# Optimization experiments

Hardware: AMD Instinct MI355X
Metric: run time of the kernel (lower is better)

The kernel has to match this reference:

```python
import jax, jax.numpy as jnp
import numpy as np

CIN, COUT, K = 64, 64, 3
ALPHA = 8.3
STRIDE, PAD, DIL = 1, 1, 1
B, H = 8, 128


def _unfold(x, k, dilation, padding, stride):
    # torch.nn.functional.unfold: output feature order is (C, kh, kw)
    x = jnp.pad(x, ((0, 0), (0, 0), (padding, padding), (padding, padding)))
    b, c, h, w = x.shape
    eff = dilation * (k - 1) + 1
    oh = (h - eff) // stride + 1
    ow = (w - eff) // stride + 1
    cols = []
    for i in range(k):
        for j in range(k):
            cols.append(x[:, :, i * dilation:i * dilation + stride * oh:stride,
                              j * dilation:j * dilation + stride * ow:stride])
    p = jnp.stack(cols, axis=2)          # [B, C, k*k, oh, ow]
    return p.reshape(b, c * k * k, oh * ow)


def setup_inputs() -> dict:
    key = jax.random.key(0)
    k1, k2, k3, k4 = jax.random.split(key, 4)
    image = jax.random.normal(k1, (B, CIN, H, H), dtype=jnp.float32)
    depth = jax.random.uniform(k2, (B, 1, H, H), dtype=jnp.float32)
    weight = jax.random.normal(k3, (COUT, CIN, K, K), dtype=jnp.float32) * 0.05
    bias = jax.random.normal(k4, (COUT,), dtype=jnp.float32) * 0.05
    return {"image": image, "depth": depth, "weight": weight, "bias": bias}


def reference(image, depth, weight, bias):
    # im2col of the image: [B, L, Cin*k*k]
    patches = _unfold(image, K, DIL, PAD, STRIDE).transpose(0, 2, 1)
    b, L, _ = patches.shape
    # depth is repeat()'d to Cin channels in the original; the unfolded depth
    # columns therefore tile the single-channel patch Cin times. Exploit that:
    dpatch = _unfold(depth, K, DIL, PAD, STRIDE).transpose(0, 2, 1)  # [B, L, k*k]
    # original centre index: int((Cin*k*k)/2); within the tiled patch this is
    # position (Cin*k*k//2) % (k*k) of the single-channel patch
    centre_idx = (CIN * K * K // 2) % (K * K)
    centre = dpatch[:, :, centre_idx:centre_idx + 1]
    sim = jnp.exp(-ALPHA * jnp.abs(dpatch - centre))  # [B, L, k*k]
    # modulate per kernel offset (broadcast over channels == tiled similarity)
    modulated = patches.reshape(b, L, CIN, K * K) * sim[:, :, None, :]
    out = jnp.einsum('blck,ock->blo', modulated, weight.reshape(COUT, CIN, K * K))
    out = out + bias
    osz = (image.shape[-1] + 2 * PAD - DIL * (K - 1) - 1) // STRIDE + 1
    return out.transpose(0, 2, 1).reshape(b, COUT, osz, osz)
```

## Files before the change

### kernel.cpp

```cpp
#include <hip/hip_runtime.h>
#include <hip/hip_bf16.h>

#define BATCH 8
#define CIN   64
#define COUT  64
#define HH    128
#define WW    128
#define ALPHA 8.3f
#define TPX   64
#define YPB   4
#define XW    66

typedef __attribute__((ext_vector_type(8))) short short8;
typedef __attribute__((ext_vector_type(4))) float f32x4;

__device__ __forceinline__ int img_idx(int r, int x, int c) {
    return (((r * XW + x) << 6) + c) ^ ((x & 7) << 3);
}

__global__ __launch_bounds__(256)
void transpose_w(const float* __restrict__ w, __hip_bfloat16* __restrict__ wt) {
    int i = blockIdx.x * 256 + threadIdx.x;
    if (i >= 9 * 64 * 64) return;
    int c = i & 63;
    int o = (i >> 6) & 63;
    int tap = i >> 12;
    wt[i] = __float2bfloat16(w[(o * 64 + c) * 9 + tap]);
}

__global__ __launch_bounds__(256)
void depthconv_mfma(const float* __restrict__ image,
                    const float* __restrict__ depth,
                    const float* __restrict__ bias,
                    const short* __restrict__ wt,
                    float* __restrict__ out) {
    __shared__ short s_img[3 * XW * 64];
    __shared__ float s_d[3][XW];
    __shared__ float s_sim[9][TPX];

    const int tid = threadIdx.x;
    const int bid = blockIdx.x;
    const int yg = bid & 31;
    const int xt = (bid >> 5) & 1;
    const int b  = bid >> 6;
    const int x0 = xt * TPX;

    const int lane = tid & 63;
    const int wid  = tid >> 6;
    const int l15  = lane & 15;
    const int lq   = lane >> 4;
    const int o_base = wid * 16;

    short8 wfrag[9][2];
    #pragma unroll
    for (int tap = 0; tap < 9; ++tap)
        #pragma unroll
        for (int h = 0; h < 2; ++h)
            wfrag[tap][h] = *(const short8*)&wt[(tap * 64 + o_base + l15) * 64 + h * 32 + lq * 8];

    float bias_v[4];
    #pragma unroll
    for (int r = 0; r < 4; ++r) bias_v[r] = bias[o_base + lq * 4 + r];

    for (int yi = 0; yi < YPB; ++yi) {
        const int y = yg * YPB + yi;
        __syncthreads();

        for (int i = tid; i < 3 * XW * 32; i += 256) {
            int x  = i % XW;
            int rr = (i / XW) % 3;
            int c  = (i / (3 * XW)) * 2;
            int gy = y + rr - 1, gx = x0 - 1 + x;
            float v0 = 0.f, v1 = 0.f;
            if ((unsigned)gy < HH && (unsigned)gx < WW) {
                const float* p = &image[((b * CIN + c) * HH + gy) * WW + gx];
                v0 = p[0];
                v1 = p[HH * WW];
            }
            __hip_bfloat162 pk = __float22bfloat162_rn(float2{v0, v1});
            *(__hip_bfloat162*)&s_img[img_idx(rr, x, c)] = pk;
        }
        for (int i = tid; i < 3 * XW; i += 256) {
            int x = i % XW, rr = i / XW;
            int gy = y + rr - 1, gx = x0 - 1 + x;
            float v = 0.f;
            if ((unsigned)gy < HH && (unsigned)gx < WW)
                v = depth[(b * HH + gy) * WW + gx];
            s_d[rr][x] = v;
        }
        __syncthreads();

        for (int i = tid; i < 9 * TPX; i += 256) {
            int p = i & 63, tap = i >> 6;
            int ri = tap / 3, dj = tap % 3;
            float dt = s_d[ri][p + dj];
            float dc = s_d[0][p];
            s_sim[tap][p] = __expf(-ALPHA * fabsf(dt - dc));
        }
        __syncthreads();

        f32x4 acc[4];
        #pragma unroll
        for (int nt = 0; nt < 4; ++nt) acc[nt] = f32x4{0.f, 0.f, 0.f, 0.f};

        #pragma unroll
        for (int tap = 0; tap < 9; ++tap) {
            const int ri = tap / 3, dj = tap % 3;
            float sv[4];
            #pragma unroll
            for (int nt = 0; nt < 4; ++nt) sv[nt] = s_sim[tap][nt * 16 + l15];
            #pragma unroll
            for (int nt = 0; nt < 4; ++nt) {
                const int xi = nt * 16 + l15 + dj;
                short8 b0 = *(const short8*)&s_img[img_idx(ri, xi, lq * 8)];
                f32x4 tmp = __builtin_amdgcn_mfma_f32_16x16x32_bf16(
                    wfrag[tap][0], b0, (f32x4){0.f, 0.f, 0.f, 0.f}, 0, 0, 0);
                short8 b1 = *(const short8*)&s_img[img_idx(ri, xi, 32 + lq * 8)];
                tmp = __builtin_amdgcn_mfma_f32_16x16x32_bf16(
                    wfrag[tap][1], b1, tmp, 0, 0, 0);
                #pragma unroll
                for (int r = 0; r < 4; ++r)
                    acc[nt][r] = fmaf(sv[nt], tmp[r], acc[nt][r]);
            }
        }

        #pragma unroll
        for (int nt = 0; nt < 4; ++nt) {
            int px = x0 + nt * 16 + l15;
            #pragma unroll
            for (int r = 0; r < 4; ++r) {
                int o = o_base + lq * 4 + r;
                out[((b * COUT + o) * HH + y) * WW + px] = acc[nt][r] + bias_v[r];
            }
        }
    }
}

extern "C" void kernel_launch(void* const* d_in, const int* in_sizes, int n_in,
                              void* d_out, int out_size, void* d_ws, size_t ws_size,
                              hipStream_t stream) {
    const float* image  = (const float*)d_in[0];
    const float* depth  = (const float*)d_in[1];
    const float* weight = (const float*)d_in[2];
    const float* bias   = (const float*)d_in[3];
    float* out = (float*)d_out;
    __hip_bfloat16* wt = (__hip_bfloat16*)d_ws;

    transpose_w<<<(9 * 64 * 64 + 255) / 256, 256, 0, stream>>>(weight, wt);

    dim3 grid(BATCH * 2 * (HH / YPB));
    depthconv_mfma<<<grid, 256, 0, stream>>>(image, depth, bias,
                                             (const short*)wt, out);
}
```

Measured before the change: 134.3 us.

## Fuse weight transpose into conv kernel and load a 4-row halo once per block

The separate weight-transpose kernel is removed; each wave now reads fp32 weights directly with float4 loads and converts them to bf16 fragments in registers. Each block now computes 2 output rows from a single 4-row image halo staged once, rather than restaging 3 rows for every output row, which cuts redundant global loads and barriers. The image staging loop is restructured so each thread streams channels for one fixed pixel, with separate handling for edge columns, and occupancy is hinted at 4 blocks per CU. The cost is more blocks each re-reading weights from global memory, plus larger shared-memory and register footprints.

```diff
diff --git a/kernel.cpp b/kernel.cpp
--- a/kernel.cpp
+++ b/kernel.cpp
@@ -6,9 +6,10 @@
 #define COUT  64
 #define HH    128
 #define WW    128
+#define HW    (HH * WW)
 #define ALPHA 8.3f
 #define TPX   64
-#define YPB   4
+#define YPB   2
 #define XW    66
 
 typedef __attribute__((ext_vector_type(8))) short short8;
@@ -18,32 +19,23 @@
     return (((r * XW + x) << 6) + c) ^ ((x & 7) << 3);
 }
 
-__global__ __launch_bounds__(256)
-void transpose_w(const float* __restrict__ w, __hip_bfloat16* __restrict__ wt) {
-    int i = blockIdx.x * 256 + threadIdx.x;
-    if (i >= 9 * 64 * 64) return;
-    int c = i & 63;
-    int o = (i >> 6) & 63;
-    int tap = i >> 12;
-    wt[i] = __float2bfloat16(w[(o * 64 + c) * 9 + tap]);
-}
-
-__global__ __launch_bounds__(256)
-void depthconv_mfma(const float* __restrict__ image,
-                    const float* __restrict__ depth,
-                    const float* __restrict__ bias,
-                    const short* __restrict__ wt,
-                    float* __restrict__ out) {
-    __shared__ short s_img[3 * XW * 64];
-    __shared__ float s_d[3][XW];
-    __shared__ float s_sim[9][TPX];
+__global__ __launch_bounds__(256, 4)
+void depthconv_fused(const float* __restrict__ image,
+                     const float* __restrict__ depth,
+                     const float* __restrict__ weight,
+                     const float* __restrict__ bias,
+                     float* __restrict__ out) {
+    __shared__ short s_img[4 * XW * 64];
+    __shared__ float s_d[4][XW];
+    __shared__ float s_sim[YPB][9][TPX];
 
     const int tid = threadIdx.x;
     const int bid = blockIdx.x;
-    const int yg = bid & 31;
-    const int xt = (bid >> 5) & 1;
-    const int b  = bid >> 6;
+    const int yg = bid & 63;
+    const int xt = (bid >> 6) & 1;
+    const int b  = bid >> 7;
     const int x0 = xt * TPX;
+    const int y0 = yg * YPB;
 
     const int lane = tid & 63;
     const int wid  = tid >> 6;
@@ -52,53 +44,85 @@
     const int o_base = wid * 16;
 
     short8 wfrag[9][2];
-    #pragma unroll
-    for (int tap = 0; tap < 9; ++tap)
+    {
+        const int o = o_base + l15;
         #pragma unroll
-        for (int h = 0; h < 2; ++h)
-            wfrag[tap][h] = *(const short8*)&wt[(tap * 64 + o_base + l15) * 64 + h * 32 + lq * 8];
+        for (int h = 0; h < 2; ++h) {
+            const float* wp = &weight[(o * CIN + h * 32 + lq * 8) * 9];
+            #pragma unroll
+            for (int q4 = 0; q4 < 18; ++q4) {
+                float4 f = *(const float4*)&wp[q4 * 4];
+                #pragma unroll
+                for (int e = 0; e < 4; ++e) {
+                    const int q  = q4 * 4 + e;
+                    const int cj = q / 9, tap = q % 9;
+                    const float fe = (e == 0) ? f.x : (e == 1) ? f.y : (e == 2) ? f.z : f.w;
+                    wfrag[tap][h][cj] =
+                        __builtin_bit_cast(short, __float2bfloat16(fe));
+                }
+            }
+        }
+    }
 
     float bias_v[4];
     #pragma unroll
     for (int r = 0; r < 4; ++r) bias_v[r] = bias[o_base + lq * 4 + r];
 
-    for (int yi = 0; yi < YPB; ++yi) {
-        const int y = yg * YPB + yi;
-        __syncthreads();
+    {
+        const int sx  = 1 + (tid & 63);
+        const int srr = tid >> 6;
+        const int gy  = y0 - 1 + srr;
+        const int gx  = x0 + (tid & 63);
+        const bool yok = (unsigned)gy < HH;
+        const float* ip = &image[((b * CIN) * HH + gy) * WW + gx];
+        const int base = (srr * XW + sx) << 6;
+        const int swz  = (sx & 7) << 3;
+        #pragma unroll 8
+        for (int c2 = 0; c2 < 32; ++c2) {
+            float v0 = 0.f, v1 = 0.f;
+            if (yok) { v0 = ip[0]; v1 = ip[HW]; }
+            ip += 2 * HW;
+            __hip_bfloat162 pk = __float22bfloat162_rn(float2{v0, v1});
+            *(__hip_bfloat162*)&s_img[base + ((2 * c2) ^ swz)] = pk;
+        }
+    }
+    {
+        const int e   = tid & 1;
+        const int sx  = e ? (XW - 1) : 0;
+        const int rr  = (tid >> 1) & 3;
+        const int c2  = tid >> 3;
+        const int gy  = y0 - 1 + rr;
+        const int gx  = x0 - 1 + sx;
+        float v0 = 0.f, v1 = 0.f;
+        if ((unsigned)gy < HH && (unsigned)gx < WW) {
+            const float* p = &image[((b * CIN + 2 * c2) * HH + gy) * WW + gx];
+            v0 = p[0]; v1 = p[HW];
+        }
+        __hip_bfloat162 pk = __float22bfloat162_rn(float2{v0, v1});
+        *(__hip_bfloat162*)&s_img[img_idx(rr, sx, 2 * c2)] = pk;
+    }
+    for (int i = tid; i < 4 * XW; i += 256) {
+        int rr = i / XW, x = i - rr * XW;
+        int gy = y0 - 1 + rr, gx = x0 - 1 + x;
+        float v = 0.f;
+        if ((unsigned)gy < HH && (unsigned)gx < WW)
+            v = depth[(b * HH + gy) * WW + gx];
+        s_d[rr][x] = v;
+    }
+    __syncthreads();
 
-        for (int i = tid; i < 3 * XW * 32; i += 256) {
-            int x  = i % XW;
-            int rr = (i / XW) % 3;
-            int c  = (i / (3 * XW)) * 2;
-            int gy = y + rr - 1, gx = x0 - 1 + x;
-            float v0 = 0.f, v1 = 0.f;
-            if ((unsigned)gy < HH && (unsigned)gx < WW) {
-                const float* p = &image[((b * CIN + c) * HH + gy) * WW + gx];
-                v0 = p[0];
-                v1 = p[HH * WW];
-            }
-            __hip_bfloat162 pk = __float22bfloat162_rn(float2{v0, v1});
-            *(__hip_bfloat162*)&s_img[img_idx(rr, x, c)] = pk;
-        }
-        for (int i = tid; i < 3 * XW; i += 256) {
-            int x = i % XW, rr = i / XW;
-            int gy = y + rr - 1, gx = x0 - 1 + x;
-            float v = 0.f;
-            if ((unsigned)gy < HH && (unsigned)gx < WW)
-                v = depth[(b * HH + gy) * WW + gx];
-            s_d[rr][x] = v;
-        }
-        __syncthreads();
+    for (int i = tid; i < YPB * 9 * TPX; i += 256) {
+        int p  = i & 63;
+        int t  = i >> 6;
+        int yy = t / 9, tap = t - yy * 9;
+        int ri = tap / 3, dj = tap - ri * 3;
+        float dt = s_d[yy + ri][p + dj];
+        float dc = s_d[yy][p];
+        s_sim[yy][tap][p] = __expf(-ALPHA * fabsf(dt - dc));
+    }
+    __syncthreads();
 
-        for (int i = tid; i < 9 * TPX; i += 256) {
-            int p = i & 63, tap = i >> 6;
-            int ri = tap / 3, dj = tap % 3;
-            float dt = s_d[ri][p + dj];
-            float dc = s_d[0][p];
-            s_sim[tap][p] = __expf(-ALPHA * fabsf(dt - dc));
-        }
-        __syncthreads();
-
+    for (int yy = 0; yy < YPB; ++yy) {
         f32x4 acc[4];
         #pragma unroll
         for (int nt = 0; nt < 4; ++nt) acc[nt] = f32x4{0.f, 0.f, 0.f, 0.f};
@@ -106,30 +130,29 @@
         #pragma unroll
         for (int tap = 0; tap < 9; ++tap) {
             const int ri = tap / 3, dj = tap % 3;
-            float sv[4];
-            #pragma unroll
-            for (int nt = 0; nt < 4; ++nt) sv[nt] = s_sim[tap][nt * 16 + l15];
             #pragma unroll
             for (int nt = 0; nt < 4; ++nt) {
                 const int xi = nt * 16 + l15 + dj;
-                short8 b0 = *(const short8*)&s_img[img_idx(ri, xi, lq * 8)];
+                short8 b0 = *(const short8*)&s_img[img_idx(yy + ri, xi, lq * 8)];
                 f32x4 tmp = __builtin_amdgcn_mfma_f32_16x16x32_bf16(
                     wfrag[tap][0], b0, (f32x4){0.f, 0.f, 0.f, 0.f}, 0, 0, 0);
-                short8 b1 = *(const short8*)&s_img[img_idx(ri, xi, 32 + lq * 8)];
+                short8 b1 = *(const short8*)&s_img[img_idx(yy + ri, xi, 32 + lq * 8)];
                 tmp = __builtin_amdgcn_mfma_f32_16x16x32_bf16(
                     wfrag[tap][1], b1, tmp, 0, 0, 0);
+                const float sv = s_sim[yy][tap][nt * 16 + l15];
                 #pragma unroll
                 for (int r = 0; r < 4; ++r)
-                    acc[nt][r] = fmaf(sv[nt], tmp[r], acc[nt][r]);
+                    acc[nt][r] = fmaf(sv, tmp[r], acc[nt][r]);
             }
         }
 
+        const int y = y0 + yy;
         #pragma unroll
         for (int nt = 0; nt < 4; ++nt) {
-            int px = x0 + nt * 16 + l15;
+            const int px = x0 + nt * 16 + l15;
             #pragma unroll
             for (int r = 0; r < 4; ++r) {
-                int o = o_base + lq * 4 + r;
+                const int o = o_base + lq * 4 + r;
                 out[((b * COUT + o) * HH + y) * WW + px] = acc[nt][r] + bias_v[r];
             }
         }
@@ -144,11 +167,7 @@
     const float* weight = (const float*)d_in[2];
     const float* bias   = (const float*)d_in[3];
     float* out = (float*)d_out;
-    __hip_bfloat16* wt = (__hip_bfloat16*)d_ws;
 
-    transpose_w<<<(9 * 64 * 64 + 255) / 256, 256, 0, stream>>>(weight, wt);
-
-    dim3 grid(BATCH * 2 * (HH / YPB));
-    depthconv_mfma<<<grid, 256, 0, stream>>>(image, depth, bias,
-                                             (const short*)wt, out);
+    dim3 grid(BATCH * (HH / YPB) * (WW / TPX));
+    depthconv_fused<<<grid, 256, 0, stream>>>(image, depth, weight, bias, out);
 }
```

Measured after the change: 162.5 us. 1.21x slower.
